# Kernel optimization log

Measured on AMD Instinct MI355X. Metric: run time of the kernel, lower is better.

Reference implementation:

```python
import jax, jax.numpy as jnp
import numpy as np

V1, V2, V3 = 20, 40, 40           # vocab factors for num_embeddings=32000
D1, D2, D3 = 4, 4, 8              # dim factors, product = embedding_dim = 128
R = 4                             # tt_rank
B, S = 32, 4096
VOCAB = V1 * V2 * V3


def _make_cores(key):
    k1, k2, k3 = jax.random.split(key, 3)
    c1 = jax.random.normal(k1, (1, V1, D1, R), dtype=jnp.float32) * 0.1
    c2 = jax.random.normal(k2, (R, V2, D2, R), dtype=jnp.float32) * 0.1
    c3 = jax.random.normal(k3, (R, V3, D3, 1), dtype=jnp.float32) * 0.1
    return c1, c2, c3


def setup_inputs() -> dict:
    key = jax.random.key(0)
    kid, kr, ki = jax.random.split(key, 3)
    input_ids = jax.random.randint(kid, (B, S), 0, 32000, dtype=jnp.int64)
    cr1, cr2, cr3 = _make_cores(kr)
    ci1, ci2, ci3 = _make_cores(ki)
    return {"input_ids": input_ids,
            "cr1": cr1, "cr2": cr2, "cr3": cr3,
            "ci1": ci1, "ci2": ci2, "ci3": ci3}


def _factors(indices):
    idx = indices % (V1 * V2 * V3)
    k = idx % V3
    idx = idx // V3
    j = idx % V2
    i = idx // V2
    return i, j, k


def _tt_half(c1, c2, c3, i, j, k):
    # gather cores per token: move vocab axis to front, index
    g1 = jnp.transpose(c1, (1, 0, 2, 3))[i][:, 0]      # [N, D1, R]  (r_in=1 squeezed)
    g2 = jnp.transpose(c2, (1, 0, 2, 3))[j]            # [N, R, D2, R]
    g3 = jnp.transpose(c3, (1, 0, 2, 3))[k][..., 0]    # [N, R, D3]  (r_out=1 squeezed)
    temp = jnp.einsum('ndr,nrfs->ndfs', g1, g2)        # [N, D1, D2, R]
    final = jnp.einsum('ndfs,nse->ndfe', temp, g3)     # [N, D1, D2, D3]
    return final.reshape(-1, D1 * D2 * D3)             # [N, 128]


def reference(input_ids, cr1, cr2, cr3, ci1, ci2, ci3):
    b, s = input_ids.shape
    i, j, k = _factors(input_ids.reshape(-1))
    real = _tt_half(cr1, cr2, cr3, i, j, k)
    imag = _tt_half(ci1, ci2, ci3, i, j, k)
    out = jnp.concatenate([real, imag], axis=-1)       # [N, 256]
    return out.reshape(b, s, 2 * D1 * D2 * D3)
```

## Files before the change

kernel.cpp:

```cpp
#include <hip/hip_runtime.h>


#define V1 20
#define V2 40
#define V3 40
#define D1 4
#define D2 4
#define D3 8
#define RNK 4

#define C1_SZ (V1*D1*RNK)
#define C2_SZ (RNK*V2*D2*RNK)
#define C3_SZ (RNK*V3*D3)
#define HALF_SZ (C1_SZ + C2_SZ + C3_SZ)
#define IMAG_OFF (HALF_SZ + 16)
#define LDS_FLOATS (IMAG_OFF + HALF_SZ)

#define TPW 16
#define BLOCK 512

__global__ __launch_bounds__(BLOCK, 8) void tt_embed_kernel(
    const int* __restrict__ ids,
    const float* __restrict__ cr1, const float* __restrict__ cr2, const float* __restrict__ cr3,
    const float* __restrict__ ci1, const float* __restrict__ ci2, const float* __restrict__ ci3,
    float* __restrict__ out, int N)
{
    __shared__ __align__(16) float lds[LDS_FLOATS];

    {
        float4*       l4r = (float4*)lds;
        float4*       l4i = (float4*)(lds + IMAG_OFF);
        const float4* s1r = (const float4*)cr1; const float4* s1i = (const float4*)ci1;
        const float4* s2r = (const float4*)cr2; const float4* s2i = (const float4*)ci2;
        const float4* s3r = (const float4*)cr3; const float4* s3i = (const float4*)ci3;
        for (int idx = threadIdx.x; idx < C1_SZ/4; idx += BLOCK) {
            l4r[idx] = s1r[idx];
            l4i[idx] = s1i[idx];
        }
        for (int idx = threadIdx.x; idx < C2_SZ/4; idx += BLOCK) {
            l4r[C1_SZ/4 + idx] = s2r[idx];
            l4i[C1_SZ/4 + idx] = s2i[idx];
        }
        for (int idx = threadIdx.x; idx < C3_SZ/4; idx += BLOCK) {
            l4r[(C1_SZ+C2_SZ)/4 + idx] = s3r[idx];
            l4i[(C1_SZ+C2_SZ)/4 + idx] = s3i[idx];
        }
    }
    __syncthreads();

    const int lane = threadIdx.x & 63;
    const int half = lane >> 5;
    const int q    = lane & 31;
    const int d    = q >> 3;
    const int f    = (q >> 1) & 3;
    const int e0   = (q & 1) * 4;

    const float* base = lds + half * IMAG_OFF;
    const float* B1 = base + d * RNK;
    const float* B2 = base + C1_SZ + f * RNK;
    const float* B3 = base + C1_SZ + C2_SZ + e0;

    const int wid = blockIdx.x * (BLOCK / 64) + (threadIdx.x >> 6);
    const int t0  = wid * TPW;

    int packed = 0;
    if (lane < TPW) {
        const int t = t0 + lane;
        if (t < N) {
            const int id = ids[t];
            const int k  = id % V3;
            const int ij = id / V3;
            const int j  = ij % V2;
            const int i  = ij / V2;
            packed = (i * (D1*RNK)) | ((j * (D2*RNK)) << 9) | ((k * D3) << 19);
        }
    }

    float* outp = out + (size_t)t0 * 256 + lane * 4;

    #pragma unroll 1
    for (int it = 0; it < TPW; ++it) {
        if (t0 + it >= N) break;
        const int p  = __builtin_amdgcn_readlane(packed, it);
        const int io = p & 0x1ff;
        const int jo = (p >> 9) & 0x3ff;
        const int ko = (p >> 19);

        const float4 g1 = *reinterpret_cast<const float4*>(B1 + io);

        const float* p2 = B2 + jo;
        const float4 a0 = *reinterpret_cast<const float4*>(p2);
        const float4 a1 = *reinterpret_cast<const float4*>(p2 +     V2*D2*RNK);
        const float4 a2 = *reinterpret_cast<const float4*>(p2 + 2 * V2*D2*RNK);
        const float4 a3 = *reinterpret_cast<const float4*>(p2 + 3 * V2*D2*RNK);
        const float tmp0 = g1.x*a0.x + g1.y*a1.x + g1.z*a2.x + g1.w*a3.x;
        const float tmp1 = g1.x*a0.y + g1.y*a1.y + g1.z*a2.y + g1.w*a3.y;
        const float tmp2 = g1.x*a0.z + g1.y*a1.z + g1.z*a2.z + g1.w*a3.z;
        const float tmp3 = g1.x*a0.w + g1.y*a1.w + g1.z*a2.w + g1.w*a3.w;

        const float* p3 = B3 + ko;
        const float4 b0 = *reinterpret_cast<const float4*>(p3);
        const float4 b1 = *reinterpret_cast<const float4*>(p3 +     V3*D3);
        const float4 b2 = *reinterpret_cast<const float4*>(p3 + 2 * V3*D3);
        const float4 b3 = *reinterpret_cast<const float4*>(p3 + 3 * V3*D3);
        float4 o;
        o.x = tmp0*b0.x + tmp1*b1.x + tmp2*b2.x + tmp3*b3.x;
        o.y = tmp0*b0.y + tmp1*b1.y + tmp2*b2.y + tmp3*b3.y;
        o.z = tmp0*b0.z + tmp1*b1.z + tmp2*b2.z + tmp3*b3.z;
        o.w = tmp0*b0.w + tmp1*b1.w + tmp2*b2.w + tmp3*b3.w;

        *reinterpret_cast<float4*>(outp) = o;
        outp += 256;
    }
}

extern "C" void kernel_launch(void* const* d_in, const int* in_sizes, int n_in,
                              void* d_out, int out_size, void* d_ws, size_t ws_size,
                              hipStream_t stream) {
    const int*   ids = (const int*)d_in[0];
    const float* cr1 = (const float*)d_in[1];
    const float* cr2 = (const float*)d_in[2];
    const float* cr3 = (const float*)d_in[3];
    const float* ci1 = (const float*)d_in[4];
    const float* ci2 = (const float*)d_in[5];
    const float* ci3 = (const float*)d_in[6];
    float* out = (float*)d_out;

    const int N = in_sizes[0];
    const int tokens_per_block = (BLOCK / 64) * TPW;
    const int blocks = (N + tokens_per_block - 1) / tokens_per_block;

    tt_embed_kernel<<<blocks, BLOCK, 0, stream>>>(ids, cr1, cr2, cr3, ci1, ci2, ci3, out, N);
}
```

Measured before the change: 30.57 us.

## Precompute first two TT core products into workspace table, gather in main kernel

Adds a small precompute kernel that contracts cores 1 and 2 for every (i,j) pair into an 800x128 table in workspace. The main kernel then reads one float4 from that table per token and does only the final rank contraction with core 3 held in LDS. This removes the per-token first contraction and shrinks LDS staging to core 3, which should help occupancy. The cost is an extra kernel launch, a global write and read of about 400 KB, and a dependence on the workspace being large enough, with the old direct kernel kept as the fallback.

```diff
diff --git a/kernel.cpp b/kernel.cpp
--- a/kernel.cpp
+++ b/kernel.cpp
@@ -9,6 +9,103 @@
 #define D3 8
 #define RNK 4
 
+#define NIJ (V1*V2)
+#define PROW 128
+#define P_BYTES (NIJ*PROW*4)
+
+__global__ __launch_bounds__(256) void tt_precompute_kernel(
+    const float* __restrict__ cr1, const float* __restrict__ cr2,
+    const float* __restrict__ ci1, const float* __restrict__ ci2,
+    float* __restrict__ P)
+{
+    const int tid = blockIdx.x * 256 + threadIdx.x;
+    if (tid >= NIJ * PROW) return;
+    const int x  = tid & 63;
+    const int h  = (tid >> 6) & 1;
+    const int ij = tid >> 7;
+    const int d = x >> 4, f = (x >> 2) & 3, s = x & 3;
+    const int i = ij / V2, j = ij - i * V2;
+    const float* c1 = h ? ci1 : cr1;
+    const float* c2 = h ? ci2 : cr2;
+    float acc = 0.f;
+    #pragma unroll
+    for (int r = 0; r < RNK; ++r)
+        acc += c1[(i*D1 + d)*RNK + r] * c2[((r*V2 + j)*D2 + f)*RNK + s];
+    P[tid] = acc;
+}
+
+#define G3_HALF (RNK*V3*D3)
+#define G3_IOFF (G3_HALF + 16)
+#define G3_LDS  (G3_IOFF + G3_HALF)
+
+#define TPW 16
+#define BLOCK 512
+
+__global__ __launch_bounds__(BLOCK, 8) void tt_gather_kernel(
+    const int* __restrict__ ids, const float* __restrict__ P,
+    const float* __restrict__ cr3, const float* __restrict__ ci3,
+    float* __restrict__ out, int N)
+{
+    __shared__ __align__(16) float g3[G3_LDS];
+    {
+        float4* l4 = (float4*)g3;
+        const float4* s3r = (const float4*)cr3;
+        const float4* s3i = (const float4*)ci3;
+        for (int idx = threadIdx.x; idx < G3_HALF/4; idx += BLOCK) {
+            l4[idx]             = s3r[idx];
+            l4[G3_IOFF/4 + idx] = s3i[idx];
+        }
+    }
+    __syncthreads();
+
+    const int lane = threadIdx.x & 63;
+    const int h    = lane >> 5;
+    const int q    = lane & 31;
+    const int e0   = (q & 1) * 4;
+
+    const float* Plane = P + h*64 + (q >> 1)*4;
+    const float* B3    = g3 + h*G3_IOFF + e0;
+
+    const int wid = blockIdx.x * (BLOCK/64) + (threadIdx.x >> 6);
+    const int t0  = wid * TPW;
+    if (t0 >= N) return;
+    const int nv = (N - t0 < TPW) ? (N - t0) : TPW;
+
+    int packed = 0;
+    if (lane < nv) {
+        const int id = ids[t0 + lane];
+        const int k  = id % V3;
+        const int ij = id / V3;
+        packed = ij | ((k * D3) << 10);
+    }
+
+    float* outp = out + (size_t)t0 * 256 + lane * 4;
+
+    #pragma unroll 1
+    for (int it = 0; it < nv; ++it) {
+        const int p  = __builtin_amdgcn_readlane(packed, it);
+        const int ij = p & 0x3ff;
+        const int k8 = p >> 10;
+
+        const float4 Pr = *reinterpret_cast<const float4*>(Plane + ij * PROW);
+
+        const float* b  = B3 + k8;
+        const float4 b0 = *reinterpret_cast<const float4*>(b);
+        const float4 b1 = *reinterpret_cast<const float4*>(b +     V3*D3);
+        const float4 b2 = *reinterpret_cast<const float4*>(b + 2 * V3*D3);
+        const float4 b3 = *reinterpret_cast<const float4*>(b + 3 * V3*D3);
+
+        float4 o;
+        o.x = Pr.x*b0.x + Pr.y*b1.x + Pr.z*b2.x + Pr.w*b3.x;
+        o.y = Pr.x*b0.y + Pr.y*b1.y + Pr.z*b2.y + Pr.w*b3.y;
+        o.z = Pr.x*b0.z + Pr.y*b1.z + Pr.z*b2.z + Pr.w*b3.z;
+        o.w = Pr.x*b0.w + Pr.y*b1.w + Pr.z*b2.w + Pr.w*b3.w;
+
+        *reinterpret_cast<float4*>(outp) = o;
+        outp += 256;
+    }
+}
+
 #define C1_SZ (V1*D1*RNK)
 #define C2_SZ (RNK*V2*D2*RNK)
 #define C3_SZ (RNK*V3*D3)
@@ -16,35 +113,22 @@
 #define IMAG_OFF (HALF_SZ + 16)
 #define LDS_FLOATS (IMAG_OFF + HALF_SZ)
 
-#define TPW 16
-#define BLOCK 512
-
-__global__ __launch_bounds__(BLOCK, 8) void tt_embed_kernel(
+__global__ __launch_bounds__(BLOCK, 8) void tt_embed_direct_kernel(
     const int* __restrict__ ids,
     const float* __restrict__ cr1, const float* __restrict__ cr2, const float* __restrict__ cr3,
     const float* __restrict__ ci1, const float* __restrict__ ci2, const float* __restrict__ ci3,
     float* __restrict__ out, int N)
 {
     __shared__ __align__(16) float lds[LDS_FLOATS];
-
     {
         float4*       l4r = (float4*)lds;
         float4*       l4i = (float4*)(lds + IMAG_OFF);
         const float4* s1r = (const float4*)cr1; const float4* s1i = (const float4*)ci1;
         const float4* s2r = (const float4*)cr2; const float4* s2i = (const float4*)ci2;
         const float4* s3r = (const float4*)cr3; const float4* s3i = (const float4*)ci3;
-        for (int idx = threadIdx.x; idx < C1_SZ/4; idx += BLOCK) {
-            l4r[idx] = s1r[idx];
-            l4i[idx] = s1i[idx];
-        }
-        for (int idx = threadIdx.x; idx < C2_SZ/4; idx += BLOCK) {
-            l4r[C1_SZ/4 + idx] = s2r[idx];
-            l4i[C1_SZ/4 + idx] = s2i[idx];
-        }
-        for (int idx = threadIdx.x; idx < C3_SZ/4; idx += BLOCK) {
-            l4r[(C1_SZ+C2_SZ)/4 + idx] = s3r[idx];
-            l4i[(C1_SZ+C2_SZ)/4 + idx] = s3i[idx];
-        }
+        for (int idx = threadIdx.x; idx < C1_SZ/4; idx += BLOCK) { l4r[idx] = s1r[idx]; l4i[idx] = s1i[idx]; }
+        for (int idx = threadIdx.x; idx < C2_SZ/4; idx += BLOCK) { l4r[C1_SZ/4+idx] = s2r[idx]; l4i[C1_SZ/4+idx] = s2i[idx]; }
+        for (int idx = threadIdx.x; idx < C3_SZ/4; idx += BLOCK) { l4r[(C1_SZ+C2_SZ)/4+idx] = s3r[idx]; l4i[(C1_SZ+C2_SZ)/4+idx] = s3i[idx]; }
     }
     __syncthreads();
 
@@ -62,32 +146,29 @@
 
     const int wid = blockIdx.x * (BLOCK / 64) + (threadIdx.x >> 6);
     const int t0  = wid * TPW;
+    if (t0 >= N) return;
+    const int nv = (N - t0 < TPW) ? (N - t0) : TPW;
 
     int packed = 0;
-    if (lane < TPW) {
-        const int t = t0 + lane;
-        if (t < N) {
-            const int id = ids[t];
-            const int k  = id % V3;
-            const int ij = id / V3;
-            const int j  = ij % V2;
-            const int i  = ij / V2;
-            packed = (i * (D1*RNK)) | ((j * (D2*RNK)) << 9) | ((k * D3) << 19);
-        }
+    if (lane < nv) {
+        const int id = ids[t0 + lane];
+        const int k  = id % V3;
+        const int ij = id / V3;
+        const int j  = ij % V2;
+        const int i  = ij / V2;
+        packed = (i * (D1*RNK)) | ((j * (D2*RNK)) << 9) | ((k * D3) << 19);
     }
 
     float* outp = out + (size_t)t0 * 256 + lane * 4;
 
     #pragma unroll 1
-    for (int it = 0; it < TPW; ++it) {
-        if (t0 + it >= N) break;
+    for (int it = 0; it < nv; ++it) {
         const int p  = __builtin_amdgcn_readlane(packed, it);
         const int io = p & 0x1ff;
         const int jo = (p >> 9) & 0x3ff;
         const int ko = (p >> 19);
 
         const float4 g1 = *reinterpret_cast<const float4*>(B1 + io);
-
         const float* p2 = B2 + jo;
         const float4 a0 = *reinterpret_cast<const float4*>(p2);
         const float4 a1 = *reinterpret_cast<const float4*>(p2 +     V2*D2*RNK);
@@ -130,5 +211,11 @@
     const int tokens_per_block = (BLOCK / 64) * TPW;
     const int blocks = (N + tokens_per_block - 1) / tokens_per_block;
 
-    tt_embed_kernel<<<blocks, BLOCK, 0, stream>>>(ids, cr1, cr2, cr3, ci1, ci2, ci3, out, N);
-}
+    if (ws_size >= (size_t)P_BYTES) {
+        float* P = (float*)d_ws;
+        tt_precompute_kernel<<<(NIJ*PROW + 255)/256, 256, 0, stream>>>(cr1, cr2, ci1, ci2, P);
+        tt_gather_kernel<<<blocks, BLOCK, 0, stream>>>(ids, P, cr3, ci3, out, N);
+    } else {
+        tt_embed_direct_kernel<<<blocks, BLOCK, 0, stream>>>(ids, cr1, cr2, cr3, ci1, ci2, ci3, out, N);
+    }
+}
```

New measurement: 33.23 us. 8.7% more time.
